# Kernel tuning notes

Hardware: AMD Instinct MI355X
Metric: run time of the kernel (lower is better)

Reference implementation:

```python
import jax, jax.numpy as jnp
import numpy as np

B, L, HID = 8, 1025, 1024
H, KV, DH = 16, 4, 64
EPS = 1e-6
ROPE_BASE = 10000.0


def _rms_norm(x, w):
    var = jnp.mean(jnp.square(x), axis=-1, keepdims=True)
    return x * jax.lax.rsqrt(var + EPS) * w


def _rotate_half(x):
    x1, x2 = jnp.split(x, 2, axis=-1)
    return jnp.concatenate([-x2, x1], axis=-1)


def _rope_cache(seq_len, dim):
    inv_freq = 1.0 / (ROPE_BASE ** (jnp.arange(0, dim, 2, dtype=jnp.float32) / dim))
    pos = jnp.arange(seq_len, dtype=jnp.float32)
    freqs = pos[:, None] * inv_freq[None, :]            # [L_img, dim/2]
    emb = jnp.concatenate([freqs, freqs], axis=-1)       # [L_img, dim]
    return jnp.cos(emb), jnp.sin(emb)


def setup_inputs() -> dict:
    key = jax.random.key(0)
    ks = jax.random.split(key, 5)
    s_in = 1.0
    s_q = float(np.sqrt(2.0 / (HID + H * DH)))
    s_kv = float(np.sqrt(2.0 / (HID + KV * DH)))
    s_o = float(np.sqrt(2.0 / (H * DH + HID)) / np.sqrt(2.0))
    return {
        "inputs": jax.random.normal(ks[0], (B, L, HID), jnp.float32) * s_in,
        "Wq": jax.random.normal(ks[1], (H * DH, HID), jnp.float32) * s_q,
        "Wk": jax.random.normal(ks[2], (KV * DH, HID), jnp.float32) * s_kv,
        "Wv": jax.random.normal(ks[3], (KV * DH, HID), jnp.float32) * s_kv,
        "Wo": jax.random.normal(ks[4], (HID, H * DH), jnp.float32) * s_o,
        "q_norm_w": jnp.ones((DH,), jnp.float32),
        "k_norm_w": jnp.ones((DH,), jnp.float32),
    }


def reference(inputs, Wq, Wk, Wv, Wo, q_norm_w, k_norm_w):
    b, l, _ = inputs.shape
    # projections (torch Linear: x @ W.T), reshape to heads, QK RMSNorm
    q = (inputs @ Wq.T).reshape(b, l, H, DH)
    k = (inputs @ Wk.T).reshape(b, l, KV, DH)
    v = (inputs @ Wv.T).reshape(b, l, KV, DH)
    q = _rms_norm(q, q_norm_w).transpose(0, 2, 1, 3)    # [B,H,L,DH]
    k = _rms_norm(k, k_norm_w).transpose(0, 2, 1, 3)    # [B,KV,L,DH]
    v = v.transpose(0, 2, 1, 3)                          # [B,KV,L,DH]

    # RoPE only on image tokens (skip first action token)
    l_img = l - 1
    cos, sin = _rope_cache(l_img, DH)                    # [L_img, DH]
    cos = cos[None, None].astype(q.dtype)
    sin = sin[None, None].astype(q.dtype)
    q_img = q[:, :, 1:]
    k_img = k[:, :, 1:]
    q = jnp.concatenate([q[:, :, :1], q_img * cos + _rotate_half(q_img) * sin], axis=2)
    k = jnp.concatenate([k[:, :, :1], k_img * cos + _rotate_half(k_img) * sin], axis=2)

    # GQA: repeat kv heads
    rep = H // KV
    k = jnp.repeat(k, rep, axis=1)                       # [B,H,L,DH]
    v = jnp.repeat(v, rep, axis=1)

    # manual attention: NOTE no 1/sqrt(DH) scaling (faithful to source)
    scores = jnp.einsum("bhqd,bhkd->bhqk", q, k)
    attn = jax.nn.softmax(scores.astype(jnp.float32), axis=-1).astype(q.dtype)
    out = jnp.einsum("bhqk,bhkd->bhqd", attn, v)         # [B,H,L,DH]
    out = out.transpose(0, 2, 1, 3).reshape(b, l, H * DH)
    return out @ Wo.T
```

## Files before the change

### kernel.cpp

```cpp
#include <hip/hip_runtime.h>
#include <hip/hip_bf16.h>

using bf16 = __hip_bfloat16;
typedef __bf16 bf16x8 __attribute__((ext_vector_type(8)));
typedef float f32x4 __attribute__((ext_vector_type(4)));
typedef short short8 __attribute__((ext_vector_type(8)));
typedef unsigned short ushort4v __attribute__((ext_vector_type(4)));

#define MFMA16(a, b, c) __builtin_amdgcn_mfma_f32_16x16x32_bf16((a), (b), (c), 0, 0, 0)

constexpr int B_ = 8, L_ = 1025, H_ = 16, KV_ = 4;
constexpr int LKP_ = 1088;
constexpr int M_ = B_ * L_;

constexpr int NX = 8396800, NWQ = 1048576, NWK = 262144, NWV = 262144,
              NWO = 1048576;

__device__ __forceinline__ void gl_lds16(const bf16* g, bf16* l) {
  __builtin_amdgcn_global_load_lds(
      (const __attribute__((address_space(1))) void*)g,
      (__attribute__((address_space(3))) void*)l, 16, 0, 0);
}

template <int NWG>
__device__ __forceinline__ int xcd_swz(int orig) {
  constexpr int q = NWG >> 3, r = NWG & 7;
  const int x = orig & 7, idx = orig >> 3;
  return (x < r ? x * (q + 1) : r * (q + 1) + (x - r) * q) + idx;
}

__global__ __launch_bounds__(64) void detect_dtype(const unsigned short* qw_raw,
                                                   int* flag) {
  if (threadIdx.x == 0) flag[0] = (qw_raw[0] == 0x3F80) ? 0 : 1;
}

__global__ __launch_bounds__(256) void convert_f32(
    const void* s0, const void* s1, const void* s2, const void* s3,
    const void* s4,
    bf16* d0, bf16* d1, bf16* d2, bf16* d3, bf16* d4,
    const int* __restrict__ flag) {
  if (*flag == 0) return;
  const int tid = blockIdx.x * blockDim.x + threadIdx.x;
  const int stride = gridDim.x * blockDim.x;
  auto conv = [&](const void* s, bf16* d, int n) {
    const float* sf = (const float*)s;
    for (int i = tid; i < n; i += stride) d[i] = __float2bfloat16(sf[i]);
  };
  conv(s0, d0, NX);
  conv(s1, d1, NWQ);
  conv(s2, d2, NWK);
  conv(s3, d3, NWV);
  conv(s4, d4, NWO);
}

__global__ __launch_bounds__(256) void zero_pads(bf16* Kb, bf16* VT) {
  const int idx = blockIdx.x * 256 + threadIdx.x;
  const bf16 z = __float2bfloat16(0.f);
  {
    const int g = idx / 4032, rem = idx % 4032;
    const int r = rem >> 6, d = rem & 63;
    Kb[((size_t)g * LKP_ + 1025 + r) * 64 + d] = z;
  }
  {
    const int row = idx / 63, c = idx % 63;
    VT[(size_t)row * LKP_ + 1025 + c] = z;
  }
}

template <int EPI, int BM, int NT, int NWG>
__global__ __launch_bounds__(512, 1) void gemm8p(
    const bf16* __restrict__ Araw, const bf16* __restrict__ Aconv,
    const bf16* __restrict__ W0r, const bf16* __restrict__ W0c,
    const bf16* __restrict__ W1r, const bf16* __restrict__ W1c,
    const bf16* __restrict__ W2r, const bf16* __restrict__ W2c,
    void* __restrict__ O0, bf16* __restrict__ O1, bf16* __restrict__ O2,
    const void* __restrict__ qwv, const void* __restrict__ kwv,
    const int* __restrict__ flag) {
  constexpr int MSPAN = BM / 2;
  constexpr int M_REP = BM / 32;
  constexpr int LA = BM / 128;
  constexpr int AOFF_ = 0;
  constexpr int BOFF_ = BM * 128;
  constexpr int DOFF_ = BOFF_ + 32768;
  constexpr int LDSZ_ = DOFF_ + 4096;

  const int f32in = *flag;
  const int wg = xcd_swz<NWG>(blockIdx.x);
  const int m0 = (wg / NT) * BM;
  const int n0 = (wg % NT) * 256;

  const bf16* A = (EPI == 0) ? Araw : (f32in ? Aconv : Araw);
  const bf16 *Wr, *Wc;
  int nw0;
  if constexpr (EPI == 0) {
    Wr = W0r; Wc = W0c; nw0 = n0;
  } else {
    if (n0 < 1024)      { Wr = W0r; Wc = W0c; nw0 = n0; }
    else if (n0 < 1280) { Wr = W1r; Wc = W1c; nw0 = n0 - 1024; }
    else                { Wr = W2r; Wc = W2c; nw0 = n0 - 1280; }
  }
  const bf16* W = f32in ? Wc : Wr;

  __shared__ bf16 lds[LDSZ_];

  const int tid = threadIdx.x, lane = tid & 63, wid = tid >> 6;
  const int wr = wid >> 2, wc = wid & 3;
  const int lo = lane & 15, g = lane >> 4;

  const f32x4 zero4 = {0.f, 0.f, 0.f, 0.f};
  f32x4 acc[M_REP][4];
#pragma unroll
  for (int i = 0; i < M_REP; ++i)
#pragma unroll
    for (int j = 0; j < 4; ++j) acc[i][j] = zero4;

  auto stage = [&](int kt, int ks) {
    const bool dum = (kt > 15);
    const int kc = dum ? 15 : kt;
    const int buf = kt & 1;
    const int kbase = kc * 64 + ks * 32;
#pragma unroll
    for (int c = 0; c < LA; ++c) {
      const int idx8 = c * 512 + tid;
      const int band = idx8 / (BM * 2);
      const int rem = idx8 - band * (BM * 2);
      const int r = rem >> 1, hh = rem & 1;
      const int hl = hh ^ ((r >> 2) & 1);
      int xr = m0 + r; if (xr > M_ - 1) xr = M_ - 1;
      const bf16* src = A + (size_t)xr * 1024 + kbase + band * 16 + hl * 8;
      bf16* dst = dum ? &lds[DOFF_ + (size_t)tid * 8]
                      : &lds[AOFF_ + ((buf * 4 + 2 * ks) * BM) * 16 + (size_t)idx8 * 8];
      gl_lds16(src, dst);
    }
#pragma unroll
    for (int c = 0; c < 2; ++c) {
      const int idx8 = c * 512 + tid;
      const int band = idx8 >> 9;
      const int rem = idx8 & 511;
      const int r = rem >> 1, hh = rem & 1;
      const int hl = hh ^ ((r >> 2) & 1);
      const bf16* src = W + (size_t)(nw0 + r) * 1024 + kbase + band * 16 + hl * 8;
      bf16* dst = dum ? &lds[DOFF_ + (size_t)tid * 8]
                      : &lds[BOFF_ + ((buf * 4 + 2 * ks) * 256) * 16 + (size_t)idx8 * 8];
      gl_lds16(src, dst);
    }
  };

  auto phase = [&](int kt, int ks) {
    if constexpr (BM == 256) asm volatile("s_waitcnt vmcnt(8)" ::: "memory");
    else                     asm volatile("s_waitcnt vmcnt(6)" ::: "memory");
    __builtin_amdgcn_s_barrier();
    __builtin_amdgcn_sched_barrier(0);
    const int buf = kt & 1;
    const int bnd = buf * 4 + 2 * ks + (g >> 1);
    bf16x8 af[M_REP], bb[4];
#pragma unroll
    for (int i = 0; i < M_REP; ++i) {
      const int row = wr * MSPAN + i * 16 + lo;
      const int hp = (g & 1) ^ ((row >> 2) & 1);
      af[i] = *reinterpret_cast<const bf16x8*>(&lds[AOFF_ + (bnd * BM + row) * 16 + hp * 8]);
    }
#pragma unroll
    for (int j = 0; j < 4; ++j) {
      const int row = wc * 64 + j * 16 + lo;
      const int hp = (g & 1) ^ ((row >> 2) & 1);
      bb[j] = *reinterpret_cast<const bf16x8*>(&lds[BOFF_ + (bnd * 256 + row) * 16 + hp * 8]);
    }
    if (ks == 0) stage(kt + 1, 1);
    else         stage(kt + 2, 0);
    asm volatile("s_waitcnt lgkmcnt(0)" ::: "memory");
    __builtin_amdgcn_sched_barrier(0);
    __builtin_amdgcn_s_setprio(1);
#pragma unroll
    for (int i = 0; i < M_REP; ++i)
#pragma unroll
      for (int j = 0; j < 4; ++j)
        acc[i][j] = MFMA16(af[i], bb[j], acc[i][j]);
    __builtin_amdgcn_s_setprio(0);
  };

  stage(0, 0); stage(0, 1); stage(1, 0);
  for (int kt = 0; kt < 16; ++kt) {
    phase(kt, 0);
    phase(kt, 1);
  }
  asm volatile("s_waitcnt vmcnt(0)" ::: "memory");

  const bool qkreg = (EPI == 1) && (n0 + wc * 64 < 1280);
  float wv[4];
  float invf0 = 0.f, invf1 = 0.f;
  if (qkreg) {
    const void* w = (n0 + wc * 64 < 1024) ? qwv : kwv;
#pragma unroll
    for (int j = 0; j < 4; ++j) {
      float wf = f32in ? ((const float*)w)[j * 16 + lo]
                       : __bfloat162float(((const bf16*)w)[j * 16 + lo]);
      wv[j] = __bfloat162float(__float2bfloat16(wf));
    }
    constexpr float cc = -0.41524101186092029f;
    invf0 = exp2f((float)lo * cc);
    invf1 = invf0 * exp2f(16.f * cc);
  }

#pragma unroll
  for (int i = 0; i < M_REP; ++i) {
#pragma unroll
    for (int ii = 0; ii < 4; ++ii) {
      const int m = m0 + wr * MSPAN + i * 16 + g * 4 + ii;
      if (m >= M_) continue;
      const int b = m / L_;
      const int l = m % L_;
      float fv[4];
#pragma unroll
      for (int j = 0; j < 4; ++j) fv[j] = acc[i][j][ii];

      if (qkreg) {
#pragma unroll
        for (int j = 0; j < 4; ++j)
          fv[j] = __bfloat162float(__float2bfloat16(fv[j]));
        float ss = fv[0] * fv[0] + fv[1] * fv[1] + fv[2] * fv[2] + fv[3] * fv[3];
        ss += __shfl_xor(ss, 1);
        ss += __shfl_xor(ss, 2);
        ss += __shfl_xor(ss, 4);
        ss += __shfl_xor(ss, 8);
        const float r = rsqrtf(ss * (1.f / 64.f) + 1e-6f);
#pragma unroll
        for (int j = 0; j < 4; ++j) fv[j] *= r * wv[j];
        if (l > 0) {
          const float pos = (float)(l - 1);
          float sn0, cs0, sn1, cs1;
          __sincosf(pos * invf0, &sn0, &cs0);
          __sincosf(pos * invf1, &sn1, &cs1);
          const float a0 = fv[0], a2 = fv[2];
          fv[0] = a0 * cs0 - a2 * sn0;
          fv[2] = a2 * cs0 + a0 * sn0;
          const float a1 = fv[1], a3 = fv[3];
          fv[1] = a1 * cs1 - a3 * sn1;
          fv[3] = a3 * cs1 + a1 * sn1;
        }
      }

#pragma unroll
      for (int j = 0; j < 4; ++j) {
        const int n = n0 + wc * 64 + j * 16 + lo;
        const float f = fv[j];
        if constexpr (EPI == 0) {
          if (f32in) ((float*)O0)[(size_t)m * 1024 + n] = f;
          else       ((bf16*)O0)[(size_t)m * 1024 + n] = __float2bfloat16(f);
        } else {
          const bf16 v = __float2bfloat16(f);
          if (n < 1024) {
            ((bf16*)O0)[((size_t)(b * H_ + (n >> 6)) * L_ + l) * 64 + (n & 63)] = v;
          } else if (n < 1280) {
            const int c2 = n - 1024;
            O1[((size_t)(b * KV_ + (c2 >> 6)) * LKP_ + l) * 64 + (c2 & 63)] = v;
          } else {
            const int c2 = n - 1280;
            O2[((size_t)(b * KV_ + (c2 >> 6)) * 64 + (c2 & 63)) * LKP_ + l] = v;
          }
        }
      }
    }
  }
}

__global__ __launch_bounds__(512) void attn(
    const bf16* __restrict__ Q, const bf16* __restrict__ Kt,
    const bf16* __restrict__ VT, bf16* __restrict__ AO) {
  const int tid = threadIdx.x, lane = tid & 63, w = tid >> 6;
  const int lo = lane & 15, g = lane >> 4;
  const int qt = blockIdx.x, h = blockIdx.y, b = blockIdx.z;
  const int kv = h >> 2;

  __shared__ unsigned short Ks[64 * 64];
  __shared__ unsigned short Vs[64 * 64];
  __shared__ unsigned short Ps[8 * 16 * 64];

  const bf16* qbase = Q + (size_t)(b * H_ + h) * L_ * 64;
  int qrow = qt * 128 + w * 16 + lo;
  if (qrow > L_ - 1) qrow = L_ - 1;
  const bf16x8 qf0 = *reinterpret_cast<const bf16x8*>(qbase + (size_t)qrow * 64 + g * 8);
  const bf16x8 qf1 = *reinterpret_cast<const bf16x8*>(qbase + (size_t)qrow * 64 + 32 + g * 8);

  const f32x4 zero4 = {0.f, 0.f, 0.f, 0.f};
  f32x4 o[4];
  float mi = -3e38f, li = 0.f;
#pragma unroll
  for (int i = 0; i < 4; ++i) o[i] = zero4;

  const int sr = tid >> 3;
  const int scol = (tid & 7) * 8;
  const int swcol = ((tid & 7) ^ (sr & 7)) * 8;
  const bf16* kptr = Kt + ((size_t)(b * KV_ + kv) * LKP_ + sr) * 64 + scol;
  const bf16* vptr = VT + ((size_t)(b * KV_ + kv) * 64 + sr) * LKP_ + scol;

  const int sw0 = (g ^ (lo & 7)) * 8;
  const int sw1 = ((4 | g) ^ (lo & 7)) * 8;

  short8 ka = *reinterpret_cast<const short8*>(kptr);
  short8 va = *reinterpret_cast<const short8*>(vptr);

  for (int kt = 0; kt < 17; ++kt) {
    __syncthreads();
    *reinterpret_cast<short8*>(&Ks[sr * 64 + swcol]) = ka;
    *reinterpret_cast<short8*>(&Vs[sr * 64 + swcol]) = va;
    __syncthreads();

    if (kt < 16) {
      kptr += 64 * 64;
      vptr += 64;
      ka = *reinterpret_cast<const short8*>(kptr);
      va = *reinterpret_cast<const short8*>(vptr);
    }

    f32x4 s[4];
    __builtin_amdgcn_s_setprio(1);
#pragma unroll
    for (int kb = 0; kb < 4; ++kb) {
      f32x4 t = zero4;
      const bf16x8 ka0 = *reinterpret_cast<const bf16x8*>(&Ks[(kb * 16 + lo) * 64 + sw0]);
      const bf16x8 ka1 = *reinterpret_cast<const bf16x8*>(&Ks[(kb * 16 + lo) * 64 + sw1]);
      t = MFMA16(ka0, qf0, t);
      t = MFMA16(ka1, qf1, t);
      s[kb] = t;
    }
    __builtin_amdgcn_s_setprio(0);
    if (kt == 16) {
#pragma unroll
      for (int kb = 0; kb < 4; ++kb)
#pragma unroll
        for (int i = 0; i < 4; ++i)
          if (kt * 64 + kb * 16 + g * 4 + i >= L_) s[kb][i] = -1e30f;
    }

    float t0 = fmaxf(fmaxf(s[0][0], s[0][1]), fmaxf(s[0][2], s[0][3]));
    float t1 = fmaxf(fmaxf(s[1][0], s[1][1]), fmaxf(s[1][2], s[1][3]));
    float t2 = fmaxf(fmaxf(s[2][0], s[2][1]), fmaxf(s[2][2], s[2][3]));
    float t3 = fmaxf(fmaxf(s[3][0], s[3][1]), fmaxf(s[3][2], s[3][3]));
    float tm = fmaxf(fmaxf(t0, t1), fmaxf(t2, t3));
    tm = fmaxf(tm, __shfl_xor(tm, 16));
    tm = fmaxf(tm, __shfl_xor(tm, 32));
    if (!__all(tm <= mi)) {
      const float mn = fmaxf(mi, tm);
      const float sc = __expf(mi - mn);
      mi = mn;
      li *= sc;
#pragma unroll
      for (int db = 0; db < 4; ++db)
#pragma unroll
        for (int i = 0; i < 4; ++i) o[db][i] *= sc;
    }
#pragma unroll
    for (int kb = 0; kb < 4; ++kb)
#pragma unroll
      for (int i = 0; i < 4; ++i) s[kb][i] = __expf(s[kb][i] - mi);
    float p0 = (s[0][0] + s[0][1]) + (s[0][2] + s[0][3]);
    float p1 = (s[1][0] + s[1][1]) + (s[1][2] + s[1][3]);
    float p2 = (s[2][0] + s[2][1]) + (s[2][2] + s[2][3]);
    float p3 = (s[3][0] + s[3][1]) + (s[3][2] + s[3][3]);
    float ps = (p0 + p1) + (p2 + p3);
    ps += __shfl_xor(ps, 16);
    ps += __shfl_xor(ps, 32);
    li += ps;

#pragma unroll
    for (int kb = 0; kb < 4; ++kb) {
      ushort4v pk;
#pragma unroll
      for (int i = 0; i < 4; ++i)
        pk[i] = __builtin_bit_cast(unsigned short, __float2bfloat16(s[kb][i]));
      const int pblk = (2 * kb + (g >> 1)) ^ (lo & 7);
      *reinterpret_cast<ushort4v*>(&Ps[w * 1024 + lo * 64 + pblk * 8 + (g & 1) * 4]) = pk;
    }

    const bf16x8 pb0 = *reinterpret_cast<const bf16x8*>(&Ps[w * 1024 + lo * 64 + sw0]);
    const bf16x8 pb1 = *reinterpret_cast<const bf16x8*>(&Ps[w * 1024 + lo * 64 + sw1]);
    __builtin_amdgcn_s_setprio(1);
#pragma unroll
    for (int db = 0; db < 4; ++db) {
      const bf16x8 va0 = *reinterpret_cast<const bf16x8*>(&Vs[(db * 16 + lo) * 64 + sw0]);
      const bf16x8 va1 = *reinterpret_cast<const bf16x8*>(&Vs[(db * 16 + lo) * 64 + sw1]);
      o[db] = MFMA16(va0, pb0, o[db]);
      o[db] = MFMA16(va1, pb1, o[db]);
    }
    __builtin_amdgcn_s_setprio(0);
  }

  const int qr = qt * 128 + w * 16 + lo;
  if (qr < L_) {
    const float inv = 1.f / li;
    unsigned* base = (unsigned*)(AO + ((size_t)b * L_ + qr) * 1024 + h * 64);
#pragma unroll
    for (int db = 0; db < 4; ++db) {
#pragma unroll
      for (int i2 = 0; i2 < 4; i2 += 2) {
        const unsigned u0 = __builtin_bit_cast(unsigned short,
                                __float2bfloat16(o[db][i2] * inv));
        const unsigned u1 = __builtin_bit_cast(unsigned short,
                                __float2bfloat16(o[db][i2 + 1] * inv));
        base[(db * 16 + 4 * g + i2) >> 1] = u0 | (u1 << 16);
      }
    }
  }
}

extern "C" void kernel_launch(void* const* d_in, const int* in_sizes, int n_in,
                              void* d_out, int out_size, void* d_ws, size_t ws_size,
                              hipStream_t stream) {
  (void)in_sizes; (void)n_in; (void)out_size; (void)ws_size;

  char* wsb = (char*)d_ws;
  int* flagp = (int*)wsb;
  bf16* cX  = (bf16*)(wsb + 16);
  bf16* cWq = cX + NX;
  bf16* cWk = cWq + NWQ;
  bf16* cWv = cWk + NWK;
  bf16* cWo = cWv + NWV;
  bf16* Qb  = cWo + NWO;
  bf16* Kb  = Qb  + (size_t)B_ * H_ * L_ * 64;
  bf16* VTb = Kb  + (size_t)B_ * KV_ * LKP_ * 64;
  bf16* AOb = VTb + (size_t)B_ * KV_ * 64 * LKP_;

  const bf16* X  = (const bf16*)d_in[0];
  const bf16* Wq = (const bf16*)d_in[1];
  const bf16* Wk = (const bf16*)d_in[2];
  const bf16* Wv = (const bf16*)d_in[3];
  const bf16* Wo = (const bf16*)d_in[4];

  detect_dtype<<<1, 64, 0, stream>>>((const unsigned short*)d_in[5], flagp);
  convert_f32<<<2048, 256, 0, stream>>>(d_in[0], d_in[1], d_in[2], d_in[3],
                                        d_in[4], cX, cWq, cWk, cWv, cWo, flagp);
  zero_pads<<<504, 256, 0, stream>>>(Kb, VTb);

  gemm8p<1, 256, 6, 198><<<198, 512, 0, stream>>>(
      X, cX, Wq, cWq, Wk, cWk, Wv, cWv, Qb, Kb, VTb, d_in[5], d_in[6], flagp);
  attn<<<dim3(9, 16, 8), 512, 0, stream>>>(Qb, Kb, VTb, AOb);
  gemm8p<0, 128, 4, 260><<<260, 512, 0, stream>>>(
      AOb, AOb, Wo, cWo, nullptr, nullptr, nullptr, nullptr, d_out,
      nullptr, nullptr, nullptr, nullptr, flagp);
}
```

Before: 228.5 us.

## Fuse Wo fp32 conversion into new register-staged output GEMM and merge setup kernels

Replaces the templated output-projection GEMM with a dedicated 128x128-tile kernel that reads Wo directly (fp32 or bf16), converting it to bf16 in registers while staging into LDS. This removes the separate Wo conversion pass and its workspace. The dtype-detect kernel is folded into zero_pads, saving one launch, and the conversion grid shrinks. The new GEMM uses plain register-to-LDS double buffering with two syncthreads per k-step instead of the direct global-to-LDS pipeline, which may lower its own efficiency.

```diff
diff --git a/kernel.cpp b/kernel.cpp
--- a/kernel.cpp
+++ b/kernel.cpp
@@ -13,8 +13,7 @@
 constexpr int LKP_ = 1088;
 constexpr int M_ = B_ * L_;
 
-constexpr int NX = 8396800, NWQ = 1048576, NWK = 262144, NWV = 262144,
-              NWO = 1048576;
+constexpr int NX = 8396800, NWQ = 1048576, NWK = 262144, NWV = 262144;
 
 __device__ __forceinline__ void gl_lds16(const bf16* g, bf16* l) {
   __builtin_amdgcn_global_load_lds(
@@ -29,15 +28,27 @@
   return (x < r ? x * (q + 1) : r * (q + 1) + (x - r) * q) + idx;
 }
 
-__global__ __launch_bounds__(64) void detect_dtype(const unsigned short* qw_raw,
-                                                   int* flag) {
-  if (threadIdx.x == 0) flag[0] = (qw_raw[0] == 0x3F80) ? 0 : 1;
+__global__ __launch_bounds__(256) void zero_pads(bf16* Kb, bf16* VT,
+                                                 const unsigned short* qw_raw,
+                                                 int* flag) {
+  if (blockIdx.x == 0 && threadIdx.x == 0)
+    flag[0] = (qw_raw[0] == 0x3F80) ? 0 : 1;
+  const int idx = blockIdx.x * 256 + threadIdx.x;
+  const bf16 z = __float2bfloat16(0.f);
+  {
+    const int g = idx / 4032, rem = idx % 4032;
+    const int r = rem >> 6, d = rem & 63;
+    Kb[((size_t)g * LKP_ + 1025 + r) * 64 + d] = z;
+  }
+  {
+    const int row = idx / 63, c = idx % 63;
+    VT[(size_t)row * LKP_ + 1025 + c] = z;
+  }
 }
 
 __global__ __launch_bounds__(256) void convert_f32(
     const void* s0, const void* s1, const void* s2, const void* s3,
-    const void* s4,
-    bf16* d0, bf16* d1, bf16* d2, bf16* d3, bf16* d4,
+    bf16* d0, bf16* d1, bf16* d2, bf16* d3,
     const int* __restrict__ flag) {
   if (*flag == 0) return;
   const int tid = blockIdx.x * blockDim.x + threadIdx.x;
@@ -50,32 +61,18 @@
   conv(s1, d1, NWQ);
   conv(s2, d2, NWK);
   conv(s3, d3, NWV);
-  conv(s4, d4, NWO);
-}
-
-__global__ __launch_bounds__(256) void zero_pads(bf16* Kb, bf16* VT) {
-  const int idx = blockIdx.x * 256 + threadIdx.x;
-  const bf16 z = __float2bfloat16(0.f);
-  {
-    const int g = idx / 4032, rem = idx % 4032;
-    const int r = rem >> 6, d = rem & 63;
-    Kb[((size_t)g * LKP_ + 1025 + r) * 64 + d] = z;
-  }
-  {
-    const int row = idx / 63, c = idx % 63;
-    VT[(size_t)row * LKP_ + 1025 + c] = z;
-  }
-}
-
-template <int EPI, int BM, int NT, int NWG>
-__global__ __launch_bounds__(512, 1) void gemm8p(
+}
+
+template <int NT, int NWG>
+__global__ __launch_bounds__(512, 1) void gemm_qkv(
     const bf16* __restrict__ Araw, const bf16* __restrict__ Aconv,
     const bf16* __restrict__ W0r, const bf16* __restrict__ W0c,
     const bf16* __restrict__ W1r, const bf16* __restrict__ W1c,
     const bf16* __restrict__ W2r, const bf16* __restrict__ W2c,
-    void* __restrict__ O0, bf16* __restrict__ O1, bf16* __restrict__ O2,
+    bf16* __restrict__ O0, bf16* __restrict__ O1, bf16* __restrict__ O2,
     const void* __restrict__ qwv, const void* __restrict__ kwv,
     const int* __restrict__ flag) {
+  constexpr int BM = 256;
   constexpr int MSPAN = BM / 2;
   constexpr int M_REP = BM / 32;
   constexpr int LA = BM / 128;
@@ -89,16 +86,12 @@
   const int m0 = (wg / NT) * BM;
   const int n0 = (wg % NT) * 256;
 
-  const bf16* A = (EPI == 0) ? Araw : (f32in ? Aconv : Araw);
+  const bf16* A = f32in ? Aconv : Araw;
   const bf16 *Wr, *Wc;
   int nw0;
-  if constexpr (EPI == 0) {
-    Wr = W0r; Wc = W0c; nw0 = n0;
-  } else {
-    if (n0 < 1024)      { Wr = W0r; Wc = W0c; nw0 = n0; }
-    else if (n0 < 1280) { Wr = W1r; Wc = W1c; nw0 = n0 - 1024; }
-    else                { Wr = W2r; Wc = W2c; nw0 = n0 - 1280; }
-  }
+  if (n0 < 1024)      { Wr = W0r; Wc = W0c; nw0 = n0; }
+  else if (n0 < 1280) { Wr = W1r; Wc = W1c; nw0 = n0 - 1024; }
+  else                { Wr = W2r; Wc = W2c; nw0 = n0 - 1280; }
   const bf16* W = f32in ? Wc : Wr;
 
   __shared__ bf16 lds[LDSZ_];
@@ -147,8 +140,7 @@
   };
 
   auto phase = [&](int kt, int ks) {
-    if constexpr (BM == 256) asm volatile("s_waitcnt vmcnt(8)" ::: "memory");
-    else                     asm volatile("s_waitcnt vmcnt(6)" ::: "memory");
+    asm volatile("s_waitcnt vmcnt(8)" ::: "memory");
     __builtin_amdgcn_s_barrier();
     __builtin_amdgcn_sched_barrier(0);
     const int buf = kt & 1;
@@ -186,7 +178,7 @@
   }
   asm volatile("s_waitcnt vmcnt(0)" ::: "memory");
 
-  const bool qkreg = (EPI == 1) && (n0 + wc * 64 < 1280);
+  const bool qkreg = (n0 + wc * 64 < 1280);
   float wv[4];
   float invf0 = 0.f, invf1 = 0.f;
   if (qkreg) {
@@ -243,22 +235,111 @@
 #pragma unroll
       for (int j = 0; j < 4; ++j) {
         const int n = n0 + wc * 64 + j * 16 + lo;
-        const float f = fv[j];
-        if constexpr (EPI == 0) {
-          if (f32in) ((float*)O0)[(size_t)m * 1024 + n] = f;
-          else       ((bf16*)O0)[(size_t)m * 1024 + n] = __float2bfloat16(f);
+        const bf16 v = __float2bfloat16(fv[j]);
+        if (n < 1024) {
+          O0[((size_t)(b * H_ + (n >> 6)) * L_ + l) * 64 + (n & 63)] = v;
+        } else if (n < 1280) {
+          const int c2 = n - 1024;
+          O1[((size_t)(b * KV_ + (c2 >> 6)) * LKP_ + l) * 64 + (c2 & 63)] = v;
         } else {
-          const bf16 v = __float2bfloat16(f);
-          if (n < 1024) {
-            ((bf16*)O0)[((size_t)(b * H_ + (n >> 6)) * L_ + l) * 64 + (n & 63)] = v;
-          } else if (n < 1280) {
-            const int c2 = n - 1024;
-            O1[((size_t)(b * KV_ + (c2 >> 6)) * LKP_ + l) * 64 + (c2 & 63)] = v;
-          } else {
-            const int c2 = n - 1280;
-            O2[((size_t)(b * KV_ + (c2 >> 6)) * 64 + (c2 & 63)) * LKP_ + l] = v;
-          }
+          const int c2 = n - 1280;
+          O2[((size_t)(b * KV_ + (c2 >> 6)) * 64 + (c2 & 63)) * LKP_ + l] = v;
         }
+      }
+    }
+  }
+}
+
+template <int NT, int NWG>
+__global__ __launch_bounds__(512) void gemm_o(
+    const bf16* __restrict__ A, const void* __restrict__ Wraw,
+    void* __restrict__ O0, const int* __restrict__ flag) {
+  const int f32in = *flag;
+  const int wg = xcd_swz<NWG>(blockIdx.x);
+  const int m0 = (wg / NT) * 128;
+  const int n0 = (wg % NT) * 128;
+
+  __shared__ bf16 As[2][128 * 32];
+  __shared__ bf16 Bs[2][128 * 32];
+
+  const int tid = threadIdx.x;
+  const int lane = tid & 63, wid = tid >> 6;
+  const int wr = wid >> 1, wc = wid & 1;
+  const int lo = lane & 15, g = lane >> 4;
+
+  const f32x4 zero4 = {0.f, 0.f, 0.f, 0.f};
+  f32x4 acc[2][4];
+#pragma unroll
+  for (int i = 0; i < 2; ++i)
+#pragma unroll
+    for (int j = 0; j < 4; ++j) acc[i][j] = zero4;
+
+  const int rr = tid >> 2, cb = tid & 3;
+  const int wofs = rr * 32 + ((cb ^ ((rr >> 1) & 3)) * 8);
+  int xr = m0 + rr; if (xr > M_ - 1) xr = M_ - 1;
+  const bf16* xp = A + (size_t)xr * 1024 + cb * 8;
+  const char* wp = (const char*)Wraw + ((size_t)(n0 + rr) * 1024 + cb * 8) * (f32in ? 4 : 2);
+  const int wstep = f32in ? 128 : 64;
+
+  f32x4 ra0, rb0, rb1;
+  auto loadA = [&] { ra0 = *(const f32x4*)xp; xp += 32; };
+  auto loadB = [&] {
+    rb0 = *(const f32x4*)wp;
+    if (f32in) rb1 = *(const f32x4*)(wp + 16);
+    wp += wstep;
+  };
+  auto packB = [&]() -> short8 {
+    if (f32in) {
+      short8 o;
+#pragma unroll
+      for (int e = 0; e < 4; ++e) {
+        o[e]     = __builtin_bit_cast(short, __float2bfloat16(rb0[e]));
+        o[e + 4] = __builtin_bit_cast(short, __float2bfloat16(rb1[e]));
+      }
+      return o;
+    }
+    return __builtin_bit_cast(short8, rb0);
+  };
+
+  loadA(); loadB();
+
+  const int swl = (g ^ ((lo >> 1) & 3)) * 8;
+
+  for (int kt = 0; kt < 32; ++kt) {
+    const int cur = kt & 1;
+    __syncthreads();
+    *reinterpret_cast<short8*>(&As[cur][wofs]) = __builtin_bit_cast(short8, ra0);
+    *reinterpret_cast<short8*>(&Bs[cur][wofs]) = packB();
+    __syncthreads();
+
+    if (kt < 31) { loadA(); loadB(); }
+
+    bf16x8 a[2], bb[4];
+#pragma unroll
+    for (int i = 0; i < 2; ++i)
+      a[i] = *reinterpret_cast<const bf16x8*>(&As[cur][(wr * 32 + i * 16 + lo) * 32 + swl]);
+#pragma unroll
+    for (int j = 0; j < 4; ++j)
+      bb[j] = *reinterpret_cast<const bf16x8*>(&Bs[cur][(wc * 64 + j * 16 + lo) * 32 + swl]);
+#pragma unroll
+    for (int i = 0; i < 2; ++i)
+#pragma unroll
+      for (int j = 0; j < 4; ++j)
+        acc[i][j] = MFMA16(a[i], bb[j], acc[i][j]);
+  }
+
+#pragma unroll
+  for (int i = 0; i < 2; ++i) {
+#pragma unroll
+    for (int ii = 0; ii < 4; ++ii) {
+      const int m = m0 + wr * 32 + i * 16 + g * 4 + ii;
+      if (m >= M_) continue;
+#pragma unroll
+      for (int j = 0; j < 4; ++j) {
+        const int n = n0 + wc * 64 + j * 16 + lo;
+        const float f = acc[i][j][ii];
+        if (f32in) ((float*)O0)[(size_t)m * 1024 + n] = f;
+        else       ((bf16*)O0)[(size_t)m * 1024 + n] = __float2bfloat16(f);
       }
     }
   }
@@ -415,8 +496,7 @@
   bf16* cWq = cX + NX;
   bf16* cWk = cWq + NWQ;
   bf16* cWv = cWk + NWK;
-  bf16* cWo = cWv + NWV;
-  bf16* Qb  = cWo + NWO;
+  bf16* Qb  = cWv + NWV;
   bf16* Kb  = Qb  + (size_t)B_ * H_ * L_ * 64;
   bf16* VTb = Kb  + (size_t)B_ * KV_ * LKP_ * 64;
   bf16* AOb = VTb + (size_t)B_ * KV_ * 64 * LKP_;
@@ -425,17 +505,14 @@
   const bf16* Wq = (const bf16*)d_in[1];
   const bf16* Wk = (const bf16*)d_in[2];
   const bf16* Wv = (const bf16*)d_in[3];
-  const bf16* Wo = (const bf16*)d_in[4];
-
-  detect_dtype<<<1, 64, 0, stream>>>((const unsigned short*)d_in[5], flagp);
-  convert_f32<<<2048, 256, 0, stream>>>(d_in[0], d_in[1], d_in[2], d_in[3],
-                                        d_in[4], cX, cWq, cWk, cWv, cWo, flagp);
-  zero_pads<<<504, 256, 0, stream>>>(Kb, VTb);
-
-  gemm8p<1, 256, 6, 198><<<198, 512, 0, stream>>>(
+
+  zero_pads<<<504, 256, 0, stream>>>(Kb, VTb, (const unsigned short*)d_in[5],
+                                     flagp);
+  convert_f32<<<512, 256, 0, stream>>>(d_in[0], d_in[1], d_in[2], d_in[3],
+                                       cX, cWq, cWk, cWv, flagp);
+
+  gemm_qkv<6, 198><<<198, 512, 0, stream>>>(
       X, cX, Wq, cWq, Wk, cWk, Wv, cWv, Qb, Kb, VTb, d_in[5], d_in[6], flagp);
   attn<<<dim3(9, 16, 8), 512, 0, stream>>>(Qb, Kb, VTb, AOb);
-  gemm8p<0, 128, 4, 260><<<260, 512, 0, stream>>>(
-      AOb, AOb, Wo, cWo, nullptr, nullptr, nullptr, nullptr, d_out,
-      nullptr, nullptr, nullptr, nullptr, flagp);
-}
+  gemm_o<8, 520><<<520, 512, 0, stream>>>(AOb, d_in[4], d_out, flagp);
+}
```

Measured after the change: 233.0 us. About the same (+2.0%).
